# Kernel tuning notes

Measured on AMD Instinct MI355X. Metric: run time of the kernel, lower is better.

## Reference

```python
import jax, jax.numpy as jnp
import numpy as np


def _fo_pool(f, z):
    # c_t = f_t * c_{t-1} + z_t, c_0 = 0, scanned over axis 1 (seq).
    # Associative combine: (a1,b1) * (a2,b2) = (a1*a2, a2*b1 + b2)
    def combine(left, right):
        a1, b1 = left
        a2, b2 = right
        return a1 * a2, a2 * b1 + b2
    _, c = jax.lax.associative_scan(combine, (f, z), axis=1)
    return c


def setup_inputs() -> dict:
    key = jax.random.key(0)
    ks = jax.random.split(key, 10)
    B, S, D_in, D_model, D_mlp, n_cls = 32, 2048, 512, 1024, 1024, 128
    s = 0.02
    return {
        "x":  jax.random.normal(ks[0], (B, S, D_in), dtype=jnp.float32),
        "W":  jax.random.normal(ks[1], (D_in, 3 * D_model), dtype=jnp.float32) * s,  # Linear, bias=False
        "V":  jax.random.normal(ks[2], (D_in, 3 * D_model), dtype=jnp.float32) * s,
        "Vb": jax.random.normal(ks[3], (3 * D_model,), dtype=jnp.float32) * s,
        "W0": jax.random.normal(ks[4], (D_model, D_mlp), dtype=jnp.float32) * s,
        "b0": jax.random.normal(ks[5], (D_mlp,), dtype=jnp.float32) * s,
        "W1": jax.random.normal(ks[6], (D_mlp, D_mlp), dtype=jnp.float32) * s,
        "b1": jax.random.normal(ks[7], (D_mlp,), dtype=jnp.float32) * s,
        "W2": jax.random.normal(ks[8], (D_mlp, n_cls), dtype=jnp.float32) * s,
        "b2": jax.random.normal(ks[9], (n_cls,), dtype=jnp.float32) * s,
    }


def reference(x, W, V, Vb, W0, b0, W1, b1, W2, b2):
    # kernel_size=2 pre: W(x) + V(x shifted right by one, zero-padded)
    xprev = jnp.pad(x[:, :-1, :], ((0, 0), (1, 0), (0, 0)))  # [B,S,D_in]
    pre = jnp.einsum('bsd,dk->bsk', x, W) + jnp.einsum('bsd,dk->bsk', xprev, V) + Vb
    f, z, o = jnp.split(pre, 3, axis=-1)
    f = jax.nn.sigmoid(f)
    z = (1.0 - f) * jnp.tanh(z)
    o = jax.nn.sigmoid(o)
    c = _fo_pool(f, z)          # [B,S,D_model]
    h = c * o
    q = h[:, -1, :]             # last timestep
    # dropout is identity at inference (training=False)
    q = jax.nn.relu(q @ W0 + b0)
    q = jax.nn.relu(q @ W1 + b1)
    return q @ W2 + b2
```

## Files before the change

### kernel.cpp

```cpp
#include <hip/hip_runtime.h>
#include <cstdint>
#include <cstddef>


typedef __attribute__((ext_vector_type(8))) short short8;
typedef __attribute__((ext_vector_type(4))) float f32x4;

#define ZERO_OFF_E 6291456u
#define XB_OFF_E   8388608u
#define U_LDS_BASE 8256

__device__ __forceinline__ unsigned short f2bf(float f) {
  unsigned int u = __float_as_uint(f);
  u += 0x7fffu + ((u >> 16) & 1u);
  return (unsigned short)(u >> 16);
}

__device__ __forceinline__ unsigned stage_addr(int r, int c) {
  return (unsigned)(r * 64 + (((c + r + (r >> 2)) & 3) << 4));
}

__device__ __forceinline__ float sigmoidf_fast(float x) {
  return 1.f / (1.f + __expf(-x));
}
__device__ __forceinline__ float tanhf_fast(float x) {
  float a = fabsf(x);
  float e = __expf(-2.f * a);
  float t = (1.f - e) / (1.f + e);
  return copysignf(t, x);
}

__device__ __forceinline__ void gload_lds16(const void* g, const char* lds) {
  __builtin_amdgcn_global_load_lds(
      (const __attribute__((address_space(1))) void*)(uintptr_t)g,
      (__attribute__((address_space(3))) void*)(uint32_t)(uintptr_t)lds, 16, 0, 0);
}

__global__ void prologue_kernel(const float* __restrict__ x, const float* __restrict__ W,
                                const float* __restrict__ V,
                                const float* __restrict__ b0, const float* __restrict__ b1,
                                const float* __restrict__ b2,
                                unsigned short* __restrict__ xb, unsigned short* __restrict__ U,
                                float* __restrict__ q0, float* __restrict__ q1,
                                float* __restrict__ out, uint4* __restrict__ zpg) {
  __shared__ float T[64 * 65];
  const int bx = blockIdx.x;
  if (bx < 8192) {
    int base = bx * 1024 + threadIdx.x;
#pragma unroll
    for (int i = 0; i < 4; ++i) {
      int gid = base + i * 256;
      float4 v = ((const float4*)x)[gid];
      ushort4 o;
      o.x = f2bf(v.x); o.y = f2bf(v.y); o.z = f2bf(v.z); o.w = f2bf(v.w);
      ((ushort4*)xb)[gid] = o;
    }
  } else if (bx < 8704) {
    const int u = bx - 8192;
    const int j0 = (u & 31) * 64;
    const int k0 = (u >> 5) * 64;
    const int jl = threadIdx.x & 63;
    const int q  = threadIdx.x >> 6;
    const float* src = (k0 < 512) ? (W + (size_t)k0 * 3072) : (V + (size_t)(k0 - 512) * 3072);
#pragma unroll 4
    for (int i = 0; i < 16; ++i) {
      int kl = q * 16 + i;
      T[kl * 65 + jl] = src[(size_t)kl * 3072 + j0 + jl];
    }
    __syncthreads();
    const int kl = threadIdx.x & 63;
#pragma unroll 4
    for (int i = 0; i < 16; ++i) {
      int jj = q * 16 + i;
      U[(size_t)(j0 + jj) * 1024 + k0 + kl] = f2bf(T[kl * 65 + jj]);
    }
  } else if (bx < 8832) {
    int gid = (bx - 8704) * 256 + threadIdx.x;
    q0[gid] = b0[gid & 1023];
    q1[gid] = b1[gid & 1023];
    if (gid < 4096) out[gid] = b2[gid & 127];
  } else {
    zpg[threadIdx.x] = make_uint4(0u, 0u, 0u, 0u);
  }
}

__global__ __launch_bounds__(512, 2) void qrnn_main8(
    const unsigned short* __restrict__ wsb, const float* __restrict__ Vb,
    float* __restrict__ Fagg, float* __restrict__ Zagg) {
  __shared__ __align__(16) char smem[131072];

  const int dt = blockIdx.x;
  const int cj = blockIdx.y;
  const int b  = blockIdx.z;
  const int tid = threadIdx.x;
  const int lane = tid & 63;
  const int wid  = tid >> 6;
  const int wm = wid >> 2, wn = wid & 3;
  const int l15 = lane & 15, lc = lane >> 4;
  const int s0 = cj * 256;

  f32x4 acc[8][4];
#pragma unroll
  for (int i = 0; i < 8; ++i)
#pragma unroll
    for (int j = 0; j < 4; ++j) acc[i][j] = f32x4{0.f, 0.f, 0.f, 0.f};

  unsigned eAx[2], eAp[2], eB[2];
#pragma unroll
  for (int i = 0; i < 2; ++i) {
    int row_g = wid * 32 + i * 16 + (lane >> 2);
    int q = (lane & 3) ^ ((row_g >> 1) & 3);
    int tx = s0 + row_g;
    eAx[i] = XB_OFF_E + (unsigned)(b * 2048 + tx) * 512u + (unsigned)(q * 8);
    int tp = s0 - 1 + row_g;
    eAp[i] = (tp < 0) ? (ZERO_OFF_E + (unsigned)(q * 8))
                      : (XB_OFF_E + (unsigned)(b * 2048 + tp) * 512u + (unsigned)(q * 8));
    int jj = (row_g < 128) ? (dt * 128 + row_g) : (1024 + dt * 128 + (row_g - 128));
    eB[i] = (unsigned)jj * 1024u + (unsigned)(q * 8);
  }

  const unsigned swz = (unsigned)((lc ^ ((l15 >> 1) & 3)) << 4);
  const unsigned oA = (unsigned)((wm * 128 + l15) * 64) + swz;
  const unsigned oB = 16384u + (unsigned)((wn * 64 + l15) * 64) + swz;

  auto stage = [&](int kt) {
    const unsigned sbase = (unsigned)((kt & 3) << 15);
    const unsigned kaddB = (unsigned)(kt * 32);
    const unsigned kaddA = (kt < 16) ? kaddB : (unsigned)((kt - 16) * 32);
    const bool xp = (kt < 16);
#pragma unroll
    for (int i = 0; i < 2; ++i) {
      unsigned da = (unsigned)__builtin_amdgcn_readfirstlane(
          (int)(sbase + (unsigned)(wid * 2048 + i * 1024)));
      const unsigned short* src = wsb + ((xp ? eAx[i] : eAp[i]) + kaddA);
      gload_lds16(src, smem + da);
    }
#pragma unroll
    for (int i = 0; i < 2; ++i) {
      unsigned db = (unsigned)__builtin_amdgcn_readfirstlane(
          (int)(sbase + 16384u + (unsigned)(wid * 2048 + i * 1024)));
      const unsigned short* src = wsb + (eB[i] + kaddB);
      gload_lds16(src, smem + db);
    }
  };

  stage(0); stage(1); stage(2);
  asm volatile("s_waitcnt vmcnt(8)" ::: "memory");
  __builtin_amdgcn_s_barrier();
  __builtin_amdgcn_sched_barrier(0);

#pragma unroll 1
  for (int kt = 0; kt < 32; ++kt) {
    const char* buf = smem + ((kt & 3) << 15);
    short8 bfr[4], afr[4];
#pragma unroll
    for (int nt = 0; nt < 4; ++nt) bfr[nt] = *(const short8*)(buf + oB + nt * 1024);
#pragma unroll
    for (int m = 0; m < 4; ++m) afr[m] = *(const short8*)(buf + oA + m * 1024);
    if (kt < 29) stage(kt + 3);
    __builtin_amdgcn_s_barrier();
    __builtin_amdgcn_s_setprio(1);
#pragma unroll
    for (int m = 0; m < 4; ++m)
#pragma unroll
      for (int nt = 0; nt < 4; ++nt)
        acc[m][nt] = __builtin_amdgcn_mfma_f32_16x16x32_bf16(afr[m], bfr[nt], acc[m][nt], 0, 0, 0);
    __builtin_amdgcn_s_setprio(0);
    __builtin_amdgcn_s_barrier();
#pragma unroll
    for (int m = 0; m < 4; ++m) afr[m] = *(const short8*)(buf + oA + (m + 4) * 1024);
    __builtin_amdgcn_s_barrier();
    __builtin_amdgcn_s_setprio(1);
#pragma unroll
    for (int m = 0; m < 4; ++m)
#pragma unroll
      for (int nt = 0; nt < 4; ++nt)
        acc[m + 4][nt] =
            __builtin_amdgcn_mfma_f32_16x16x32_bf16(afr[m], bfr[nt], acc[m + 4][nt], 0, 0, 0);
    __builtin_amdgcn_s_setprio(0);
    if (kt <= 28)      asm volatile("s_waitcnt vmcnt(8)" ::: "memory");
    else if (kt == 29) asm volatile("s_waitcnt vmcnt(4)" ::: "memory");
    else               asm volatile("s_waitcnt vmcnt(0)" ::: "memory");
    __builtin_amdgcn_s_barrier();
    __builtin_amdgcn_sched_barrier(0);
  }

  float* fA   = (float*)smem;
  float* tzA  = (float*)(smem + 33792);
  float* segF = (float*)(smem + 67584);
  float* segZ = (float*)(smem + 69632);

  float vb[4];
#pragma unroll
  for (int nt = 0; nt < 4; ++nt)
    vb[nt] = Vb[(wn >> 1) * 1024 + dt * 128 + (wn & 1) * 64 + nt * 16 + l15];

  const int d = tid & 127;
  const int seg = tid >> 7;
  float F_run = 1.f, Z_run = 0.f;

#pragma unroll
  for (int ph = 0; ph < 4; ++ph) {
    __syncthreads();
    if (wm == (ph >> 1)) {
      float* dst = (wn < 2) ? fA : tzA;
#pragma unroll
      for (int m = 0; m < 4; ++m) {
#pragma unroll
        for (int nt = 0; nt < 4; ++nt)
#pragma unroll
          for (int rg = 0; rg < 4; ++rg) {
            int t = m * 16 + (lc << 2) + rg;
            int c = (wn & 1) * 64 + nt * 16 + l15;
            float v = acc[(ph & 1) * 4 + m][nt][rg] + vb[nt];
            v = (wn < 2) ? sigmoidf_fast(v) : tanhf_fast(v);
            dst[t * 132 + c] = v;
          }
      }
    }
    __syncthreads();
    {
      float F = 1.f, Z = 0.f;
#pragma unroll 4
      for (int i = 0; i < 16; ++i) {
        int t = seg * 16 + i;
        float f  = fA[t * 132 + d];
        float tz = tzA[t * 132 + d];
        float z = (1.f - f) * tz;
        Z = f * Z + z;
        F *= f;
      }
      segF[seg * 128 + d] = F;
      segZ[seg * 128 + d] = Z;
    }
    __syncthreads();
    if (tid < 128) {
#pragma unroll
      for (int sgi = 0; sgi < 4; ++sgi) {
        float Fs = segF[sgi * 128 + tid], Zs = segZ[sgi * 128 + tid];
        Z_run = Fs * Z_run + Zs;
        F_run *= Fs;
      }
    }
  }
  if (tid < 128) {
    size_t o = (((size_t)b * 8 + cj) << 10) + dt * 128 + tid;
    Fagg[o] = F_run;
    Zagg[o] = Z_run;
  }
}

template <bool USE_BF>
__global__ __launch_bounds__(256, 3) void qrnn_main(
    const unsigned short* __restrict__ wsb, const float* __restrict__ xf,
    const float* __restrict__ Vb,
    float* __restrict__ Fagg, float* __restrict__ Zagg) {
  __shared__ __align__(16) char smem[36864];

  const int dt = blockIdx.x;
  const int cj = blockIdx.y;
  const int b  = blockIdx.z;
  const int tid = threadIdx.x;
  const int lane = tid & 63;
  const int wid  = tid >> 6;
  const int wm = wid >> 1, wn = wid & 1;
  const int s0 = cj * 128;
  const int l15 = lane & 15, lc = lane >> 4;

  f32x4 acc[4][4];
#pragma unroll
  for (int i = 0; i < 4; ++i)
#pragma unroll
    for (int j = 0; j < 4; ++j) acc[i][j] = f32x4{0.f, 0.f, 0.f, 0.f};

  unsigned voffA[2];
  size_t offAF[2]; int zAF[2];
#pragma unroll
  for (int p = 0; p < 2; ++p) {
    int cw = tid + p * 256;
    int r = cw >> 2, c = cw & 3;
    int sg = s0 - 1 + r;
    voffA[p] = (sg < 0) ? (ZERO_OFF_E + (unsigned)(c * 8))
                        : (XB_OFF_E + (unsigned)(b * 2048 + sg) * 512u + (unsigned)(c * 8));
    zAF[p] = (sg < 0);
    offAF[p] = ((size_t)(b * 2048 + (sg < 0 ? 0 : sg)) << 9) + c * 8;
  }
  unsigned voffA3 = XB_OFF_E + (unsigned)(b * 2048 + s0 + 127) * 512u + (unsigned)((tid & 3) * 8);
  size_t offAF3 = ((size_t)(b * 2048 + s0 + 127) << 9) + (tid & 3) * 8;

  unsigned voffU[4];
#pragma unroll
  for (int k = 0; k < 4; ++k) {
    int uw = tid + k * 256;
    int r = uw >> 2, c = uw & 3;
    int col = r & 127, half = r >> 7;
    int j = (col < 64) ? (dt * 64 + col) : (1024 + dt * 64 + (col - 64));
    voffU[k] = (unsigned)(j * 1024 + half * 512 + c * 8);
  }

  unsigned wA[2], wU[4];
#pragma unroll
  for (int p = 0; p < 2; ++p) {
    int cw = tid + p * 256;
    wA[p] = stage_addr(cw >> 2, cw & 3);
  }
  const unsigned wA3 = stage_addr(128, tid & 3);
#pragma unroll
  for (int k = 0; k < 4; ++k) {
    int uw = tid + k * 256;
    wU[k] = U_LDS_BASE + stage_addr(uw >> 2, uw & 3);
  }

  unsigned roA[2][4], roU[2][4];
#pragma unroll
  for (int h2 = 0; h2 < 2; ++h2) {
#pragma unroll
    for (int mt = 0; mt < 4; ++mt) {
      int rr = wm * 64 + l15 + mt * 16 + 1 - h2;
      roA[h2][mt] = stage_addr(rr, lc);
    }
#pragma unroll
    for (int nt = 0; nt < 4; ++nt) {
      int rrU = h2 * 128 + wn * 64 + l15 + nt * 16;
      roU[h2][nt] = U_LDS_BASE + stage_addr(rrU, lc);
    }
  }

  uint4 pA0, pA1, pA3, pU0, pU1, pU2, pU3;

  auto load_stage = [&](int s) {
    const unsigned short* cur = wsb + s * 32;
    if constexpr (USE_BF) {
      pA0 = *(const uint4*)(cur + voffA[0]);
      pA1 = *(const uint4*)(cur + voffA[1]);
      if (tid < 4) pA3 = *(const uint4*)(cur + voffA3);
    } else {
      const float* curf = xf + s * 32;
#pragma unroll
      for (int p = 0; p < 2; ++p) {
        uint4 v = make_uint4(0u, 0u, 0u, 0u);
        if (!zAF[p]) {
          float4 a0 = *(const float4*)(curf + offAF[p]);
          float4 a1 = *(const float4*)(curf + offAF[p] + 4);
          v.x = (unsigned)f2bf(a0.x) | ((unsigned)f2bf(a0.y) << 16);
          v.y = (unsigned)f2bf(a0.z) | ((unsigned)f2bf(a0.w) << 16);
          v.z = (unsigned)f2bf(a1.x) | ((unsigned)f2bf(a1.y) << 16);
          v.w = (unsigned)f2bf(a1.z) | ((unsigned)f2bf(a1.w) << 16);
        }
        if (p == 0) pA0 = v; else pA1 = v;
      }
      if (tid < 4) {
        float4 a0 = *(const float4*)(curf + offAF3);
        float4 a1 = *(const float4*)(curf + offAF3 + 4);
        pA3.x = (unsigned)f2bf(a0.x) | ((unsigned)f2bf(a0.y) << 16);
        pA3.y = (unsigned)f2bf(a0.z) | ((unsigned)f2bf(a0.w) << 16);
        pA3.z = (unsigned)f2bf(a1.x) | ((unsigned)f2bf(a1.y) << 16);
        pA3.w = (unsigned)f2bf(a1.z) | ((unsigned)f2bf(a1.w) << 16);
      }
    }
    pU0 = *(const uint4*)(cur + voffU[0]);
    pU1 = *(const uint4*)(cur + voffU[1]);
    pU2 = *(const uint4*)(cur + voffU[2]);
    pU3 = *(const uint4*)(cur + voffU[3]);
  };

  load_stage(0);

#pragma unroll 1
  for (int s = 0; s < 16; ++s) {
    __syncthreads();
    *(uint4*)(smem + wA[0]) = pA0;
    *(uint4*)(smem + wA[1]) = pA1;
    if (tid < 4) *(uint4*)(smem + wA3) = pA3;
    *(uint4*)(smem + wU[0]) = pU0;
    *(uint4*)(smem + wU[1]) = pU1;
    *(uint4*)(smem + wU[2]) = pU2;
    *(uint4*)(smem + wU[3]) = pU3;
    __syncthreads();
    if (s < 15) load_stage(s + 1);
#pragma unroll
    for (int h2 = 0; h2 < 2; ++h2) {
      short8 bfr[4];
#pragma unroll
      for (int nt = 0; nt < 4; ++nt)
        bfr[nt] = *(const short8*)(smem + roU[h2][nt]);
#pragma unroll
      for (int mt = 0; mt < 4; ++mt) {
        short8 afr = *(const short8*)(smem + roA[h2][mt]);
#pragma unroll
        for (int nt = 0; nt < 4; ++nt)
          acc[mt][nt] = __builtin_amdgcn_mfma_f32_16x16x32_bf16(afr, bfr[nt], acc[mt][nt], 0, 0, 0);
      }
    }
  }

  float* fA   = (float*)smem;
  float* tzA  = (float*)(smem + 17408);
  float* segF = (float*)(smem + 34816);
  float* segZ = (float*)(smem + 35840);

  const int d = tid & 63;
  float vb[4];
#pragma unroll
  for (int nt = 0; nt < 4; ++nt)
    vb[nt] = Vb[wn * 1024 + dt * 64 + nt * 16 + l15];

  float F_run = 1.f, Z_run = 0.f;

  for (int ph = 0; ph < 2; ++ph) {
    __syncthreads();
    if (wm == ph) {
      float* dst = (wn == 0) ? fA : tzA;
#pragma unroll
      for (int mt = 0; mt < 4; ++mt)
#pragma unroll
        for (int nt = 0; nt < 4; ++nt)
#pragma unroll
          for (int rg = 0; rg < 4; ++rg) {
            int t = mt * 16 + ((lane >> 4) << 2) + rg;
            int c = nt * 16 + l15;
            float v = acc[mt][nt][rg] + vb[nt];
            v = (wn == 0) ? sigmoidf_fast(v) : tanhf_fast(v);
            dst[t * 68 + c] = v;
          }
    }
    __syncthreads();
    {
      int seg = tid >> 6;
      float F = 1.f, Z = 0.f;
#pragma unroll 4
      for (int i = 0; i < 16; ++i) {
        int t = seg * 16 + i;
        float f  = fA[t * 68 + d];
        float tz = tzA[t * 68 + d];
        float z = (1.f - f) * tz;
        Z = f * Z + z;
        F *= f;
      }
      segF[seg * 64 + d] = F;
      segZ[seg * 64 + d] = Z;
    }
    __syncthreads();
    if (tid < 64) {
#pragma unroll
      for (int sgi = 0; sgi < 4; ++sgi) {
        float Fs = segF[sgi * 64 + tid], Zs = segZ[sgi * 64 + tid];
        Z_run = Fs * Z_run + Zs;
        F_run *= Fs;
      }
    }
  }
  if (tid < 64) {
    size_t o = (((size_t)b * 16 + cj) << 10) + dt * 64 + tid;
    Fagg[o] = F_run;
    Zagg[o] = Z_run;
  }
}

__global__ void head_kernel(const float* __restrict__ x, const float* __restrict__ W,
                            const float* __restrict__ V, const float* __restrict__ Vb,
                            const float* __restrict__ Fagg, const float* __restrict__ Zagg,
                            float* __restrict__ h, int nch) {
  __shared__ float red[4][64];
  const int dl = threadIdx.x & 63;
  const int w  = threadIdx.x >> 6;
  const int d = blockIdx.x * 64 + dl;
  const int b = blockIdx.y;

  const float* xl = x + ((size_t)b * 2048 + 2047) * 512;
  const float* xp = xl - 512;
  const float* Wc = W + 2048 + d;
  const float* Vc = V + 2048 + d;
  float po = 0.f;
  const int k0 = w * 128;
#pragma unroll 8
  for (int k = k0; k < k0 + 128; ++k) {
    po += xl[k] * Wc[(size_t)k * 3072];
    po += xp[k] * Vc[(size_t)k * 3072];
  }
  red[w][dl] = po;
  __syncthreads();
  if (w == 0) {
    po = red[0][dl] + red[1][dl] + red[2][dl] + red[3][dl] + Vb[2048 + d];
    float c = 0.f;
    for (int j = 0; j < nch; ++j) {
      size_t o = (((size_t)b * nch + j) << 10) + d;
      c = Fagg[o] * c + Zagg[o];
    }
    h[((size_t)b << 10) + d] = c * sigmoidf_fast(po);
  }
}

__global__ void mlp_atomic_kernel(const float* __restrict__ in, const float* __restrict__ Wt,
                                  float* __restrict__ out, int K, int N, int relu_in) {
  __shared__ float red[4][64];
  const int nl = threadIdx.x & 63;
  const int w  = threadIdx.x >> 6;
  const int n = blockIdx.x * 64 + nl;
  const int b = blockIdx.y;
  const int k0 = blockIdx.z * (K >> 2) + w * (K >> 4);
  const float* row = in + (size_t)b * K;
  const float* Wc = Wt + n;
  float s = 0.f;
#pragma unroll 8
  for (int k = k0; k < k0 + (K >> 4); ++k) {
    float v = row[k];
    if (relu_in) v = fmaxf(v, 0.f);
    s += v * Wc[(size_t)k * N];
  }
  red[w][nl] = s;
  __syncthreads();
  if (w == 0) {
    s = red[0][nl] + red[1][nl] + red[2][nl] + red[3][nl];
    atomicAdd(&out[(size_t)b * N + n], s);
  }
}

extern "C" void kernel_launch(void* const* d_in, const int* in_sizes, int n_in,
                              void* d_out, int out_size, void* d_ws, size_t ws_size,
                              hipStream_t stream) {
  const float* x  = (const float*)d_in[0];
  const float* W  = (const float*)d_in[1];
  const float* V  = (const float*)d_in[2];
  const float* Vb = (const float*)d_in[3];
  const float* W0 = (const float*)d_in[4];
  const float* b0 = (const float*)d_in[5];
  const float* W1 = (const float*)d_in[6];
  const float* b1 = (const float*)d_in[7];
  const float* W2 = (const float*)d_in[8];
  const float* b2 = (const float*)d_in[9];

  char* ws = (char*)d_ws;
  unsigned short* U = (unsigned short*)(ws);
  float* Fagg = (float*)(ws + (size_t)4 * 1024 * 1024);
  float* Zagg = (float*)(ws + (size_t)6 * 1024 * 1024);
  float* h    = (float*)(ws + (size_t)8 * 1024 * 1024);
  float* q0   = (float*)(ws + (size_t)8 * 1024 * 1024 + 256 * 1024);
  float* q1   = (float*)(ws + (size_t)8 * 1024 * 1024 + 512 * 1024);
  uint4* zpg  = (uint4*)(ws + (size_t)12 * 1024 * 1024);
  unsigned short* xb = (unsigned short*)(ws + (size_t)16 * 1024 * 1024);

  const size_t need_bf = (size_t)16 * 1024 * 1024 + (size_t)67108864;
  int use_bf = (ws_size >= need_bf) ? 1 : 0;

  prologue_kernel<<<8833, 256, 0, stream>>>(x, W, V, b0, b1, b2, xb, U, q0, q1,
                                            (float*)d_out, zpg);
  if (use_bf) {
    qrnn_main8<<<dim3(8, 8, 32), 512, 0, stream>>>((const unsigned short*)ws, Vb, Fagg, Zagg);
    head_kernel<<<dim3(16, 32), 256, 0, stream>>>(x, W, V, Vb, Fagg, Zagg, h, 8);
  } else {
    qrnn_main<false><<<dim3(16, 16, 32), 256, 0, stream>>>((const unsigned short*)ws, x,
                                                           Vb, Fagg, Zagg);
    head_kernel<<<dim3(16, 32), 256, 0, stream>>>(x, W, V, Vb, Fagg, Zagg, h, 16);
  }
  mlp_atomic_kernel<<<dim3(16, 32, 4), 256, 0, stream>>>(h, W0, q0, 1024, 1024, 0);
  mlp_atomic_kernel<<<dim3(16, 32, 4), 256, 0, stream>>>(q0, W1, q1, 1024, 1024, 1);
  mlp_atomic_kernel<<<dim3(2, 32, 4), 256, 0, stream>>>(q1, W2, (float*)d_out, 1024, 128, 1);
}
```

Measured before the change: 667.7 us.

## Prefetch next k-step LDS fragments, split staging, and remap blocks across XCDs

Restructures the GEMM main loop so the next k-step's A/B fragments are read from LDS while the current MFMAs run. It uses double-buffered register fragments and a macro-unrolled pair of steps. The global-to-LDS staging is split into A and B halves issued around the first MFMA batch. The grid is flattened to 1D with a block-id remap, (bid&7)*256+(bid>>3), so each XCD gets a contiguous range of tiles for better L2 locality. The extra register fragments raise register pressure at 2 blocks per CU, and the wait/barrier ordering changes.

```diff
diff --git a/kernel.cpp b/kernel.cpp
--- a/kernel.cpp
+++ b/kernel.cpp
@@ -89,9 +89,12 @@
     float* __restrict__ Fagg, float* __restrict__ Zagg) {
   __shared__ __align__(16) char smem[131072];
 
-  const int dt = blockIdx.x;
-  const int cj = blockIdx.y;
-  const int b  = blockIdx.z;
+  const int bid  = blockIdx.x;
+  const int orig = (bid & 7) * 256 + (bid >> 3);
+  const int dt = orig & 7;
+  const int cj = (orig >> 3) & 7;
+  const int b  = orig >> 6;
+
   const int tid = threadIdx.x;
   const int lane = tid & 63;
   const int wid  = tid >> 6;
@@ -123,67 +126,90 @@
   const unsigned oA = (unsigned)((wm * 128 + l15) * 64) + swz;
   const unsigned oB = 16384u + (unsigned)((wn * 64 + l15) * 64) + swz;
 
-  auto stage = [&](int kt) {
+  auto stage_half = [&](int kt, int h) {
     const unsigned sbase = (unsigned)((kt & 3) << 15);
-    const unsigned kaddB = (unsigned)(kt * 32);
-    const unsigned kaddA = (kt < 16) ? kaddB : (unsigned)((kt - 16) * 32);
-    const bool xp = (kt < 16);
-#pragma unroll
-    for (int i = 0; i < 2; ++i) {
-      unsigned da = (unsigned)__builtin_amdgcn_readfirstlane(
-          (int)(sbase + (unsigned)(wid * 2048 + i * 1024)));
-      const unsigned short* src = wsb + ((xp ? eAx[i] : eAp[i]) + kaddA);
-      gload_lds16(src, smem + da);
-    }
-#pragma unroll
-    for (int i = 0; i < 2; ++i) {
-      unsigned db = (unsigned)__builtin_amdgcn_readfirstlane(
-          (int)(sbase + 16384u + (unsigned)(wid * 2048 + i * 1024)));
-      const unsigned short* src = wsb + (eB[i] + kaddB);
-      gload_lds16(src, smem + db);
+    if (h == 0) {
+      const unsigned kaddA = (kt < 16) ? (unsigned)(kt * 32) : (unsigned)((kt - 16) * 32);
+      const bool xp = (kt < 16);
+#pragma unroll
+      for (int i = 0; i < 2; ++i) {
+        unsigned da = (unsigned)__builtin_amdgcn_readfirstlane(
+            (int)(sbase + (unsigned)(wid * 2048 + i * 1024)));
+        gload_lds16(wsb + ((xp ? eAx[i] : eAp[i]) + kaddA), smem + da);
+      }
+    } else {
+      const unsigned kaddB = (unsigned)(kt * 32);
+#pragma unroll
+      for (int i = 0; i < 2; ++i) {
+        unsigned db = (unsigned)__builtin_amdgcn_readfirstlane(
+            (int)(sbase + 16384u + (unsigned)(wid * 2048 + i * 1024)));
+        gload_lds16(wsb + (eB[i] + kaddB), smem + db);
+      }
     }
   };
 
-  stage(0); stage(1); stage(2);
+  stage_half(0, 0); stage_half(0, 1);
+  stage_half(1, 0); stage_half(1, 1);
+  stage_half(2, 0); stage_half(2, 1);
   asm volatile("s_waitcnt vmcnt(8)" ::: "memory");
   __builtin_amdgcn_s_barrier();
   __builtin_amdgcn_sched_barrier(0);
 
+  short8 bC[4], aC[4], bN[4], aN[4], aH[4];
+#pragma unroll
+  for (int nt = 0; nt < 4; ++nt) bC[nt] = *(const short8*)(smem + oB + nt * 1024);
+#pragma unroll
+  for (int m = 0; m < 4; ++m)   aC[m]  = *(const short8*)(smem + oA + m * 1024);
+
+#define KSTEP(KT, Bc, Ac, Bn, An)                                                   \
+  {                                                                                 \
+    const int kt = (KT);                                                            \
+    const char* buf  = smem + ((kt & 3) << 15);                                     \
+    const char* bufn = smem + (((kt + 1) & 3) << 15);                               \
+                   \
+    _Pragma("unroll")                                                               \
+    for (int m = 0; m < 4; ++m) aH[m] = *(const short8*)(buf + oA + (m + 4) * 1024);\
+    if (kt < 29) stage_half(kt + 3, 0);                                             \
+    __builtin_amdgcn_s_barrier();                                                   \
+    __builtin_amdgcn_s_setprio(1);                                                  \
+    _Pragma("unroll")                                                               \
+    for (int m = 0; m < 4; ++m)                                                     \
+      _Pragma("unroll")                                                             \
+      for (int nt = 0; nt < 4; ++nt)                                                \
+        acc[m][nt] =                                                                \
+            __builtin_amdgcn_mfma_f32_16x16x32_bf16(Ac[m], Bc[nt], acc[m][nt], 0, 0, 0); \
+    __builtin_amdgcn_s_setprio(0);                                                  \
+    if (kt < 29) stage_half(kt + 3, 1);                                             \
+    if (kt <= 28)      asm volatile("s_waitcnt vmcnt(8)" ::: "memory");             \
+    else if (kt == 29) asm volatile("s_waitcnt vmcnt(4)" ::: "memory");             \
+    else if (kt == 30) asm volatile("s_waitcnt vmcnt(0)" ::: "memory");             \
+    __builtin_amdgcn_s_barrier();                                                   \
+                        \
+    if (kt < 31) {                                                                  \
+      _Pragma("unroll")                                                             \
+      for (int nt = 0; nt < 4; ++nt) Bn[nt] = *(const short8*)(bufn + oB + nt * 1024); \
+      _Pragma("unroll")                                                             \
+      for (int m = 0; m < 4; ++m)   An[m]  = *(const short8*)(bufn + oA + m * 1024);\
+    }                                                                               \
+    __builtin_amdgcn_s_barrier();                                                   \
+    __builtin_amdgcn_s_setprio(1);                                                  \
+    _Pragma("unroll")                                                               \
+    for (int m = 0; m < 4; ++m)                                                     \
+      _Pragma("unroll")                                                             \
+      for (int nt = 0; nt < 4; ++nt)                                                \
+        acc[m + 4][nt] =                                                            \
+            __builtin_amdgcn_mfma_f32_16x16x32_bf16(aH[m], Bc[nt], acc[m + 4][nt], 0, 0, 0); \
+    __builtin_amdgcn_s_setprio(0);                                                  \
+    __builtin_amdgcn_s_barrier();                                                   \
+    __builtin_amdgcn_sched_barrier(0);                                              \
+  }
+
 #pragma unroll 1
-  for (int kt = 0; kt < 32; ++kt) {
-    const char* buf = smem + ((kt & 3) << 15);
-    short8 bfr[4], afr[4];
-#pragma unroll
-    for (int nt = 0; nt < 4; ++nt) bfr[nt] = *(const short8*)(buf + oB + nt * 1024);
-#pragma unroll
-    for (int m = 0; m < 4; ++m) afr[m] = *(const short8*)(buf + oA + m * 1024);
-    if (kt < 29) stage(kt + 3);
-    __builtin_amdgcn_s_barrier();
-    __builtin_amdgcn_s_setprio(1);
-#pragma unroll
-    for (int m = 0; m < 4; ++m)
-#pragma unroll
-      for (int nt = 0; nt < 4; ++nt)
-        acc[m][nt] = __builtin_amdgcn_mfma_f32_16x16x32_bf16(afr[m], bfr[nt], acc[m][nt], 0, 0, 0);
-    __builtin_amdgcn_s_setprio(0);
-    __builtin_amdgcn_s_barrier();
-#pragma unroll
-    for (int m = 0; m < 4; ++m) afr[m] = *(const short8*)(buf + oA + (m + 4) * 1024);
-    __builtin_amdgcn_s_barrier();
-    __builtin_amdgcn_s_setprio(1);
-#pragma unroll
-    for (int m = 0; m < 4; ++m)
-#pragma unroll
-      for (int nt = 0; nt < 4; ++nt)
-        acc[m + 4][nt] =
-            __builtin_amdgcn_mfma_f32_16x16x32_bf16(afr[m], bfr[nt], acc[m + 4][nt], 0, 0, 0);
-    __builtin_amdgcn_s_setprio(0);
-    if (kt <= 28)      asm volatile("s_waitcnt vmcnt(8)" ::: "memory");
-    else if (kt == 29) asm volatile("s_waitcnt vmcnt(4)" ::: "memory");
-    else               asm volatile("s_waitcnt vmcnt(0)" ::: "memory");
-    __builtin_amdgcn_s_barrier();
-    __builtin_amdgcn_sched_barrier(0);
-  }
+  for (int k2 = 0; k2 < 32; k2 += 2) {
+    KSTEP(k2,     bC, aC, bN, aN);
+    KSTEP(k2 + 1, bN, aN, bC, aC);
+  }
+#undef KSTEP
 
   float* fA   = (float*)smem;
   float* tzA  = (float*)(smem + 33792);
@@ -546,7 +572,7 @@
   prologue_kernel<<<8833, 256, 0, stream>>>(x, W, V, b0, b1, b2, xb, U, q0, q1,
                                             (float*)d_out, zpg);
   if (use_bf) {
-    qrnn_main8<<<dim3(8, 8, 32), 512, 0, stream>>>((const unsigned short*)ws, Vb, Fagg, Zagg);
+    qrnn_main8<<<2048, 512, 0, stream>>>((const unsigned short*)ws, Vb, Fagg, Zagg);
     head_kernel<<<dim3(16, 32), 256, 0, stream>>>(x, W, V, Vb, Fagg, Zagg, h, 8);
   } else {
     qrnn_main<false><<<dim3(16, 16, 32), 256, 0, stream>>>((const unsigned short*)ws, x,
```

Result: no change. 666.9 us (-0.1%).
